# Optimization experiments

Hardware: AMD Instinct MI355X
Metric: run time of the kernel (lower is better)

Reference implementation:

```python
import jax, jax.numpy as jnp
import numpy as np

N, C, H, W = 8, 256, 64, 64  # C == dim_inner

def conv1x1(x, w, b):
    # x: [N,C,H,W], w: [O,C], b: [O]  (1x1 conv == per-pixel matmul)
    return jnp.einsum('oc,nchw->nohw', w, x) + b[None, :, None, None]

def setup_inputs() -> dict:
    key = jax.random.key(0)
    ks = jax.random.split(key, 10)
    s = 1.0 / np.sqrt(C)
    return {
        'x':       jax.random.normal(ks[0], (N, C, H, W), dtype=jnp.float32),
        'w_theta': jax.random.uniform(ks[1], (C, C), jnp.float32, -s, s),
        'b_theta': jax.random.uniform(ks[2], (C,),   jnp.float32, -s, s),
        'w_phi':   jax.random.uniform(ks[3], (C, C), jnp.float32, -s, s),
        'b_phi':   jax.random.uniform(ks[4], (C,),   jnp.float32, -s, s),
        'w_g':     jax.random.uniform(ks[5], (C, C), jnp.float32, -s, s),
        'b_g':     jax.random.uniform(ks[6], (C,),   jnp.float32, -s, s),
        'w_out':   jax.random.uniform(ks[7], (C, C), jnp.float32, -s, s),
        'b_out':   jax.random.uniform(ks[8], (C,),   jnp.float32, -s, s),
        'gamma':   jnp.ones((C,), jnp.float32),
        'beta':    jnp.zeros((C,), jnp.float32),
        'w_gate':  jnp.asarray(0.5, jnp.float32),
    }

def reference(x, w_theta, b_theta, w_phi, b_phi, w_g, b_g, w_out, b_out, gamma, beta, w_gate):
    norm_eps = 1e-5
    x_identity = x
    theta = conv1x1(x, w_theta, b_theta).reshape(N, C, H * W)
    phi   = conv1x1(x, w_phi,   b_phi  ).reshape(N, C, H * W)
    g     = conv1x1(x, w_g,     b_g    ).reshape(N, C, H * W)
    # [N, HW, HW] attention scores
    theta_phi = jnp.einsum('nch,ncp->nhp', theta, phi) * (C ** -0.5)
    theta_phi = jax.nn.softmax(theta_phi, axis=2)
    theta_phi_g = jnp.einsum('nhg,ncg->nch', theta_phi, g).reshape(N, C, H, W)
    p = conv1x1(theta_phi_g, w_out, b_out)
    # BatchNorm2d in training mode: batch stats over (N,H,W), biased var
    mean = p.mean(axis=(0, 2, 3))
    var = p.var(axis=(0, 2, 3))
    p = (p - mean[None, :, None, None]) * jax.lax.rsqrt(var + norm_eps)[None, :, None, None]
    p = p * gamma[None, :, None, None] + beta[None, :, None, None]
    z = (1.0 - w_gate) * x_identity + w_gate * p
    return z
```

## Files before the change

kernel.cpp:

```cpp
#include <hip/hip_runtime.h>

#define N_ 8
#define C_ 256
#define HW_ 4096

typedef __bf16 bf16x8 __attribute__((ext_vector_type(8)));
typedef float f32x4 __attribute__((ext_vector_type(4)));
typedef unsigned short u16x8 __attribute__((ext_vector_type(8)));

#define MFMA(a, b, c) __builtin_amdgcn_mfma_f32_16x16x32_bf16(a, b, c, 0, 0, 0)

static __device__ __forceinline__ unsigned short f2bf(float f) {
    union { float f; unsigned int u; } v; v.f = f;
    unsigned int u = v.u;
    return (unsigned short)((u + 0x7FFFu + ((u >> 16) & 1u)) >> 16);
}

static __device__ __forceinline__ bf16x8 pack_bf8(float4 a, float4 b) {
    u16x8 t;
    t[0] = f2bf(a.x); t[1] = f2bf(a.y); t[2] = f2bf(a.z); t[3] = f2bf(a.w);
    t[4] = f2bf(b.x); t[5] = f2bf(b.y); t[6] = f2bf(b.z); t[7] = f2bf(b.w);
    return __builtin_bit_cast(bf16x8, t);
}

__global__ __launch_bounds__(256) void qkv_kernel(
    const float* __restrict__ x,
    const float* __restrict__ w_theta, const float* __restrict__ b_theta,
    const float* __restrict__ w_phi,   const float* __restrict__ b_phi,
    const float* __restrict__ w_g,     const float* __restrict__ b_g,
    unsigned short* __restrict__ thetaT, unsigned short* __restrict__ phiT,
    unsigned short* __restrict__ gC)
{
    __shared__ unsigned short xT[64 * 264];
    const int tid = threadIdx.x;
    const int hw0 = blockIdx.x * 64;
    const int n   = blockIdx.y;
    const float* xb = x + (size_t)n * C_ * HW_;
    for (int i = 0; i < 16; ++i) {
        int e   = tid + i * 256;
        int c   = e >> 4;
        int hw4 = (e & 15) << 2;
        float4 v = *reinterpret_cast<const float4*>(xb + (size_t)c * HW_ + hw0 + hw4);
        xT[(hw4 + 0) * 264 + c] = f2bf(v.x);
        xT[(hw4 + 1) * 264 + c] = f2bf(v.y);
        xT[(hw4 + 2) * 264 + c] = f2bf(v.z);
        xT[(hw4 + 3) * 264 + c] = f2bf(v.w);
    }
    __syncthreads();

    const int w = tid >> 6, lane = tid & 63;
    const int g16 = lane >> 4, l16 = lane & 15;

    const float* Wp[3] = { w_theta, w_phi, w_g };
    const float* Bp[3] = { b_theta, b_phi, b_g };

    for (int ot = 0; ot < 4; ++ot) {
        const int oB    = ot * 64;
        const int wrow  = oB + w * 16 + l16;
        const int orow0 = oB + w * 16 + g16 * 4;
        #pragma unroll
        for (int wt = 0; wt < 3; ++wt) {
            const float* W = Wp[wt];
            bf16x8 aw[8];
            #pragma unroll
            for (int kk = 0; kk < 8; ++kk) {
                const float* wp = W + (size_t)wrow * C_ + kk * 32 + g16 * 8;
                float4 f0 = *reinterpret_cast<const float4*>(wp);
                float4 f1 = *reinterpret_cast<const float4*>(wp + 4);
                aw[kk] = pack_bf8(f0, f1);
            }
            f32x4 acc[4];
            #pragma unroll
            for (int cb = 0; cb < 4; ++cb) {
                acc[cb][0] = 0.f; acc[cb][1] = 0.f; acc[cb][2] = 0.f; acc[cb][3] = 0.f;
            }
            #pragma unroll
            for (int kk = 0; kk < 8; ++kk) {
                #pragma unroll
                for (int cb = 0; cb < 4; ++cb) {
                    bf16x8 b = *reinterpret_cast<const bf16x8*>(
                        &xT[(cb * 16 + l16) * 264 + kk * 32 + g16 * 8]);
                    acc[cb] = MFMA(aw[kk], b, acc[cb]);
                }
            }
            const float* bp = Bp[wt];
            float bj0 = bp[orow0], bj1 = bp[orow0 + 1], bj2 = bp[orow0 + 2], bj3 = bp[orow0 + 3];
            if (wt == 2) { bj0 = 0.f; bj1 = 0.f; bj2 = 0.f; bj3 = 0.f; }
            if (wt < 2) {
                unsigned short* dst = (wt == 0) ? thetaT : phiT;
                const float sc = (wt == 0) ? 0.0625f : 1.0f;
                #pragma unroll
                for (int cb = 0; cb < 4; ++cb) {
                    int hw = hw0 + cb * 16 + l16;
                    ushort4 pk;
                    pk.x = f2bf((acc[cb][0] + bj0) * sc);
                    pk.y = f2bf((acc[cb][1] + bj1) * sc);
                    pk.z = f2bf((acc[cb][2] + bj2) * sc);
                    pk.w = f2bf((acc[cb][3] + bj3) * sc);
                    *reinterpret_cast<ushort4*>(&dst[((size_t)n * HW_ + hw) * C_ + orow0]) = pk;
                }
            } else {
                #pragma unroll
                for (int cb = 0; cb < 4; ++cb) {
                    int hw = hw0 + cb * 16 + l16;
                    gC[((size_t)n * C_ + orow0 + 0) * HW_ + hw] = f2bf(acc[cb][0]);
                    gC[((size_t)n * C_ + orow0 + 1) * HW_ + hw] = f2bf(acc[cb][1]);
                    gC[((size_t)n * C_ + orow0 + 2) * HW_ + hw] = f2bf(acc[cb][2]);
                    gC[((size_t)n * C_ + orow0 + 3) * HW_ + hw] = f2bf(acc[cb][3]);
                }
            }
        }
    }
}

__global__ __launch_bounds__(256, 2) void attn_kernel(
    const unsigned short* __restrict__ thetaT,
    const unsigned short* __restrict__ phiT,
    const unsigned short* __restrict__ gC,
    unsigned short* __restrict__ tpgT)
{
    __shared__ unsigned short Kl[64 * 264];
    __shared__ unsigned short Vl[256 * 72];
    __shared__ unsigned short Pl[4 * 16 * 72];
    const int tid = threadIdx.x;
    const int h0  = blockIdx.x * 64;
    const int n   = blockIdx.y;
    const int w = tid >> 6, lane = tid & 63, g16 = lane >> 4, l16 = lane & 15;

    bf16x8 q[8];
    {
        const unsigned short* qp = thetaT + ((size_t)n * HW_ + h0 + w * 16 + l16) * C_;
        #pragma unroll
        for (int kk = 0; kk < 8; ++kk)
            q[kk] = *reinterpret_cast<const bf16x8*>(qp + kk * 32 + g16 * 8);
    }
    f32x4 oacc[16];
    #pragma unroll
    for (int i = 0; i < 16; ++i) { oacc[i][0]=0.f; oacc[i][1]=0.f; oacc[i][2]=0.f; oacc[i][3]=0.f; }
    float mj[4] = { -1e30f, -1e30f, -1e30f, -1e30f };
    float lj[4] = { 0.f, 0.f, 0.f, 0.f };

    const unsigned short* Kb = phiT + (size_t)n * HW_ * C_;
    const unsigned short* Vb = gC   + (size_t)n * C_ * HW_;
    unsigned short* Pw = Pl + w * 16 * 72;

    for (int t = 0; t < 64; ++t) {
        __syncthreads();
        for (int i = 0; i < 8; ++i) {
            int e = tid + i * 256;
            int r = e >> 5, c8 = (e & 31) << 3;
            *reinterpret_cast<uint4*>(&Kl[r * 264 + c8]) =
                *reinterpret_cast<const uint4*>(Kb + ((size_t)t * 64 + r) * C_ + c8);
        }
        for (int i = 0; i < 8; ++i) {
            int e = tid + i * 256;
            int c = e >> 3, o8 = (e & 7) << 3;
            *reinterpret_cast<uint4*>(&Vl[c * 72 + o8]) =
                *reinterpret_cast<const uint4*>(Vb + (size_t)c * HW_ + t * 64 + o8);
        }
        __syncthreads();

        f32x4 s[4];
        #pragma unroll
        for (int cb = 0; cb < 4; ++cb) { s[cb][0]=0.f; s[cb][1]=0.f; s[cb][2]=0.f; s[cb][3]=0.f; }
        #pragma unroll
        for (int kk = 0; kk < 8; ++kk) {
            #pragma unroll
            for (int cb = 0; cb < 4; ++cb) {
                bf16x8 b = *reinterpret_cast<const bf16x8*>(
                    &Kl[(cb * 16 + l16) * 264 + kk * 32 + g16 * 8]);
                s[cb] = MFMA(q[kk], b, s[cb]);
            }
        }
        #pragma unroll
        for (int j = 0; j < 4; ++j) {
            float v0 = fmaxf(fmaxf(s[0][j], s[1][j]), fmaxf(s[2][j], s[3][j]));
            v0 = fmaxf(v0, __shfl_xor(v0, 1));
            v0 = fmaxf(v0, __shfl_xor(v0, 2));
            v0 = fmaxf(v0, __shfl_xor(v0, 4));
            v0 = fmaxf(v0, __shfl_xor(v0, 8));
            float mn = fmaxf(mj[j], v0);
            float sc = __expf(mj[j] - mn);
            float rs = 0.f;
            int r = g16 * 4 + j;
            #pragma unroll
            for (int cb = 0; cb < 4; ++cb) {
                float pv = __expf(s[cb][j] - mn);
                rs += pv;
                Pw[r * 72 + cb * 16 + l16] = f2bf(pv);
            }
            rs += __shfl_xor(rs, 1);
            rs += __shfl_xor(rs, 2);
            rs += __shfl_xor(rs, 4);
            rs += __shfl_xor(rs, 8);
            lj[j] = lj[j] * sc + rs;
            mj[j] = mn;
            #pragma unroll
            for (int ncb = 0; ncb < 16; ++ncb) oacc[ncb][j] *= sc;
        }
        #pragma unroll
        for (int k2 = 0; k2 < 2; ++k2) {
            bf16x8 pa = *reinterpret_cast<const bf16x8*>(&Pw[l16 * 72 + k2 * 32 + g16 * 8]);
            #pragma unroll
            for (int ncb = 0; ncb < 16; ++ncb) {
                bf16x8 vb = *reinterpret_cast<const bf16x8*>(
                    &Vl[(ncb * 16 + l16) * 72 + k2 * 32 + g16 * 8]);
                oacc[ncb] = MFMA(pa, vb, oacc[ncb]);
            }
        }
    }
    #pragma unroll
    for (int j = 0; j < 4; ++j) {
        float inv = 1.0f / lj[j];
        int h = h0 + w * 16 + g16 * 4 + j;
        unsigned short* op = tpgT + ((size_t)n * HW_ + h) * C_;
        #pragma unroll
        for (int ncb = 0; ncb < 16; ++ncb)
            op[ncb * 16 + l16] = f2bf(oacc[ncb][j] * inv);
    }
}

__global__ __launch_bounds__(256) void outconv_kernel(
    const unsigned short* __restrict__ tpgT,
    const float* __restrict__ w_out, const float* __restrict__ b_out,
    float* __restrict__ p, float* __restrict__ bnsum, float* __restrict__ bnsumsq)
{
    __shared__ unsigned short Bl[64 * 264];
    const int tid = threadIdx.x;
    const int hw0 = blockIdx.x * 64;
    const int n   = blockIdx.y;
    const unsigned short* Tb = tpgT + (size_t)n * HW_ * C_;
    for (int i = 0; i < 8; ++i) {
        int e = tid + i * 256;
        int r = e >> 5, c8 = (e & 31) << 3;
        *reinterpret_cast<uint4*>(&Bl[r * 264 + c8]) =
            *reinterpret_cast<const uint4*>(Tb + ((size_t)hw0 + r) * C_ + c8);
    }
    __syncthreads();
    const int w = tid >> 6, lane = tid & 63, g16 = lane >> 4, l16 = lane & 15;

    for (int ot = 0; ot < 4; ++ot) {
        const int oB   = ot * 64;
        const int wrow = oB + w * 16 + l16;
        bf16x8 aw[8];
        #pragma unroll
        for (int kk = 0; kk < 8; ++kk) {
            const float* wp = w_out + (size_t)wrow * C_ + kk * 32 + g16 * 8;
            float4 f0 = *reinterpret_cast<const float4*>(wp);
            float4 f1 = *reinterpret_cast<const float4*>(wp + 4);
            aw[kk] = pack_bf8(f0, f1);
        }
        f32x4 acc[4];
        #pragma unroll
        for (int cb = 0; cb < 4; ++cb) { acc[cb][0]=0.f; acc[cb][1]=0.f; acc[cb][2]=0.f; acc[cb][3]=0.f; }
        #pragma unroll
        for (int kk = 0; kk < 8; ++kk) {
            #pragma unroll
            for (int cb = 0; cb < 4; ++cb) {
                bf16x8 b = *reinterpret_cast<const bf16x8*>(
                    &Bl[(cb * 16 + l16) * 264 + kk * 32 + g16 * 8]);
                acc[cb] = MFMA(aw[kk], b, acc[cb]);
            }
        }
        const int orow0 = oB + w * 16 + g16 * 4;
        float bj[4] = { b_out[orow0], b_out[orow0 + 1], b_out[orow0 + 2], b_out[orow0 + 3] };
        float s1[4] = {0.f,0.f,0.f,0.f}, s2[4] = {0.f,0.f,0.f,0.f};
        #pragma unroll
        for (int cb = 0; cb < 4; ++cb) {
            #pragma unroll
            for (int j = 0; j < 4; ++j) {
                float pv = acc[cb][j] + bj[j];
                p[((size_t)n * C_ + orow0 + j) * HW_ + hw0 + cb * 16 + l16] = pv;
                s1[j] += pv;
                s2[j] += pv * pv;
            }
        }
        #pragma unroll
        for (int j = 0; j < 4; ++j) {
            float a1 = s1[j], a2 = s2[j];
            a1 += __shfl_xor(a1, 1); a2 += __shfl_xor(a2, 1);
            a1 += __shfl_xor(a1, 2); a2 += __shfl_xor(a2, 2);
            a1 += __shfl_xor(a1, 4); a2 += __shfl_xor(a2, 4);
            a1 += __shfl_xor(a1, 8); a2 += __shfl_xor(a2, 8);
            if (l16 == 0) {
                atomicAdd(&bnsum[orow0 + j], a1);
                atomicAdd(&bnsumsq[orow0 + j], a2);
            }
        }
    }
}

__global__ void bnfin_kernel(const float* __restrict__ bnsum,
                             const float* __restrict__ bnsumsq,
                             const float* __restrict__ gamma,
                             const float* __restrict__ beta,
                             float* __restrict__ bnscale, float* __restrict__ bnshift)
{
    int c = threadIdx.x;
    const float cnt = (float)(N_ * HW_);
    float mean = bnsum[c] / cnt;
    float var  = bnsumsq[c] / cnt - mean * mean;
    float inv  = rsqrtf(var + 1e-5f);
    float sc   = gamma[c] * inv;
    bnscale[c] = sc;
    bnshift[c] = beta[c] - mean * sc;
}

__global__ __launch_bounds__(256) void final_kernel(
    const float* __restrict__ x, const float* __restrict__ p,
    const float* __restrict__ bnscale, const float* __restrict__ bnshift,
    const float* __restrict__ wgate, float* __restrict__ out)
{
    const float wg = *wgate;
    const float og = 1.0f - wg;
    const int total = N_ * C_ * HW_ / 4;
    for (int e = blockIdx.x * 256 + threadIdx.x; e < total; e += gridDim.x * 256) {
        int c = (e >> 10) & 255;
        float sc = bnscale[c], sh = bnshift[c];
        float4 xv = reinterpret_cast<const float4*>(x)[e];
        float4 pv = reinterpret_cast<const float4*>(p)[e];
        float4 z;
        z.x = og * xv.x + wg * (pv.x * sc + sh);
        z.y = og * xv.y + wg * (pv.y * sc + sh);
        z.z = og * xv.z + wg * (pv.z * sc + sh);
        z.w = og * xv.w + wg * (pv.w * sc + sh);
        reinterpret_cast<float4*>(out)[e] = z;
    }
}

extern "C" void kernel_launch(void* const* d_in, const int* in_sizes, int n_in,
                              void* d_out, int out_size, void* d_ws, size_t ws_size,
                              hipStream_t stream)
{
    (void)in_sizes; (void)n_in; (void)out_size; (void)ws_size;
    const float* x       = (const float*)d_in[0];
    const float* w_theta = (const float*)d_in[1];
    const float* b_theta = (const float*)d_in[2];
    const float* w_phi   = (const float*)d_in[3];
    const float* b_phi   = (const float*)d_in[4];
    const float* w_g     = (const float*)d_in[5];
    const float* b_g     = (const float*)d_in[6];
    const float* w_out   = (const float*)d_in[7];
    const float* b_out   = (const float*)d_in[8];
    const float* gamma   = (const float*)d_in[9];
    const float* beta    = (const float*)d_in[10];
    const float* wgate   = (const float*)d_in[11];
    float* out = (float*)d_out;

    char* ws = (char*)d_ws;
    unsigned short* thetaT = (unsigned short*)(ws + 0);
    unsigned short* phiT   = (unsigned short*)(ws + 16777216);
    unsigned short* gC     = (unsigned short*)(ws + 33554432);
    unsigned short* tpgT   = (unsigned short*)(ws + 50331648);
    float* p       = (float*)(ws + 0);
    float* bnsum   = (float*)(ws + 67108864);
    float* bnsumsq = (float*)(ws + 67108864 + 1024);
    float* bnscale = (float*)(ws + 67108864 + 2048);
    float* bnshift = (float*)(ws + 67108864 + 3072);

    hipMemsetAsync(bnsum, 0, 2048, stream);

    qkv_kernel<<<dim3(64, 8), 256, 0, stream>>>(
        x, w_theta, b_theta, w_phi, b_phi, w_g, b_g, thetaT, phiT, gC);
    attn_kernel<<<dim3(64, 8), 256, 0, stream>>>(thetaT, phiT, gC, tpgT);
    outconv_kernel<<<dim3(64, 8), 256, 0, stream>>>(tpgT, w_out, b_out, p, bnsum, bnsumsq);
    bnfin_kernel<<<1, 256, 0, stream>>>(bnsum, bnsumsq, gamma, beta, bnscale, bnshift);
    final_kernel<<<dim3(2048), 256, 0, stream>>>(x, p, bnscale, bnshift, wgate, out);
}
```

Before: 582.1 us.

## Rewrite attention with 32x32 MFMA, split-KV waves, register-resident P and lazy rescale

The flash-attention kernel moves from 16x16x32 to 32x32x16 bf16 MFMA tiles and computes S transposed, so the probabilities can be packed with v_cvt_pk_bf16 and permlane32 swaps straight into the A operand of the PV MFMA, with no LDS round trip. The four waves are split into two query sub-tiles times two KV halves, each half keeping its own running max and sum, and the halves are merged through LDS at the end. Output rescaling is skipped unless the max grows by more than 8, and the block index is remapped with batch innermost. The aim is higher MFMA efficiency and less LDS and softmax overhead, at the cost of more registers, a final merge step, and some numeric slack from the lazy rescale threshold.

```diff
diff --git a/kernel.cpp b/kernel.cpp
--- a/kernel.cpp
+++ b/kernel.cpp
@@ -6,9 +6,12 @@
 
 typedef __bf16 bf16x8 __attribute__((ext_vector_type(8)));
 typedef float f32x4 __attribute__((ext_vector_type(4)));
+typedef float f32x16 __attribute__((ext_vector_type(16)));
 typedef unsigned short u16x8 __attribute__((ext_vector_type(8)));
-
-#define MFMA(a, b, c) __builtin_amdgcn_mfma_f32_16x16x32_bf16(a, b, c, 0, 0, 0)
+typedef unsigned int uint2v __attribute__((ext_vector_type(2)));
+
+#define MFMA(a, b, c)   __builtin_amdgcn_mfma_f32_16x16x32_bf16(a, b, c, 0, 0, 0)
+#define MFMA32(a, b, c) __builtin_amdgcn_mfma_f32_32x32x16_bf16(a, b, c, 0, 0, 0)
 
 static __device__ __forceinline__ unsigned short f2bf(float f) {
     union { float f; unsigned int u; } v; v.f = f;
@@ -21,6 +24,21 @@
     t[0] = f2bf(a.x); t[1] = f2bf(a.y); t[2] = f2bf(a.z); t[3] = f2bf(a.w);
     t[4] = f2bf(b.x); t[5] = f2bf(b.y); t[6] = f2bf(b.z); t[7] = f2bf(b.w);
     return __builtin_bit_cast(bf16x8, t);
+}
+
+static __device__ __forceinline__ unsigned cvt_pk_bf16(float lo, float hi) {
+    unsigned r;
+    asm("v_cvt_pk_bf16_f32 %0, %1, %2" : "=v"(r) : "v"(lo), "v"(hi));
+    return r;
+}
+
+static __device__ __forceinline__ void plswap(unsigned& a, unsigned& b) {
+#if __has_builtin(__builtin_amdgcn_permlane32_swap)
+    uint2v r = __builtin_amdgcn_permlane32_swap(a, b, false, false);
+    a = r[0]; b = r[1];
+#else
+    asm volatile("v_permlane32_swap_b32 %0, %1" : "+v"(a), "+v"(b));
+#endif
 }
 
 __global__ __launch_bounds__(256) void qkv_kernel(
@@ -119,104 +137,161 @@
     const unsigned short* __restrict__ gC,
     unsigned short* __restrict__ tpgT)
 {
-    __shared__ unsigned short Kl[64 * 264];
-    __shared__ unsigned short Vl[256 * 72];
-    __shared__ unsigned short Pl[4 * 16 * 72];
-    const int tid = threadIdx.x;
-    const int h0  = blockIdx.x * 64;
-    const int n   = blockIdx.y;
-    const int w = tid >> 6, lane = tid & 63, g16 = lane >> 4, l16 = lane & 15;
-
-    bf16x8 q[8];
-    {
-        const unsigned short* qp = thetaT + ((size_t)n * HW_ + h0 + w * 16 + l16) * C_;
-        #pragma unroll
-        for (int kk = 0; kk < 8; ++kk)
-            q[kk] = *reinterpret_cast<const bf16x8*>(qp + kk * 32 + g16 * 8);
-    }
-    f32x4 oacc[16];
-    #pragma unroll
-    for (int i = 0; i < 16; ++i) { oacc[i][0]=0.f; oacc[i][1]=0.f; oacc[i][2]=0.f; oacc[i][3]=0.f; }
-    float mj[4] = { -1e30f, -1e30f, -1e30f, -1e30f };
-    float lj[4] = { 0.f, 0.f, 0.f, 0.f };
+    __shared__ __align__(16) unsigned short smem[2 * 32 * 264 + 2 * 256 * 40];
+    __shared__ float mlds[2][2][32];
+    unsigned short* KlA = smem;
+    unsigned short* KlB = smem + 32 * 264;
+    unsigned short* VlA = smem + 2 * 32 * 264;
+    unsigned short* VlB = VlA + 256 * 40;
+
+    const int tid  = threadIdx.x;
+    const int bid  = blockIdx.x;
+    const int n    = bid & 7;
+    const int q0   = (bid >> 3) * 64;
+    const int w    = tid >> 6, lane = tid & 63;
+    const int l31  = lane & 31;
+    const int hi8  = (lane >> 5) << 3;
+    const int qsub = w & 1, kvhalf = w >> 1;
 
     const unsigned short* Kb = phiT + (size_t)n * HW_ * C_;
     const unsigned short* Vb = gC   + (size_t)n * C_ * HW_;
-    unsigned short* Pw = Pl + w * 16 * 72;
+    const unsigned short* Klh = kvhalf ? KlB : KlA;
+    const unsigned short* Vlh = kvhalf ? VlB : VlA;
+    const int kvbase0 = kvhalf * 2048;
+
+    bf16x8 qf[16];
+    {
+        const unsigned short* qp = thetaT + ((size_t)n * HW_ + q0 + qsub * 32 + l31) * C_;
+        #pragma unroll
+        for (int kk = 0; kk < 16; ++kk)
+            qf[kk] = *reinterpret_cast<const bf16x8*>(qp + kk * 16 + hi8);
+    }
+
+    f32x16 oacc[8];
+    #pragma unroll
+    for (int ncb = 0; ncb < 8; ++ncb)
+        #pragma unroll
+        for (int r = 0; r < 16; ++r) oacc[ncb][r] = 0.f;
+    float m = -1e30f, l = 0.f;
 
     for (int t = 0; t < 64; ++t) {
+        const int kvA = t * 32;
+        const int kvB = 2048 + t * 32;
         __syncthreads();
-        for (int i = 0; i < 8; ++i) {
+        #pragma unroll
+        for (int i = 0; i < 4; ++i) {
             int e = tid + i * 256;
-            int r = e >> 5, c8 = (e & 31) << 3;
-            *reinterpret_cast<uint4*>(&Kl[r * 264 + c8]) =
-                *reinterpret_cast<const uint4*>(Kb + ((size_t)t * 64 + r) * C_ + c8);
-        }
-        for (int i = 0; i < 8; ++i) {
-            int e = tid + i * 256;
-            int c = e >> 3, o8 = (e & 7) << 3;
-            *reinterpret_cast<uint4*>(&Vl[c * 72 + o8]) =
-                *reinterpret_cast<const uint4*>(Vb + (size_t)c * HW_ + t * 64 + o8);
+            int r  = e >> 5, c8 = (e & 31) << 3;
+            *reinterpret_cast<uint4*>(&KlA[r * 264 + c8]) =
+                *reinterpret_cast<const uint4*>(Kb + (size_t)(kvA + r) * C_ + c8);
+            *reinterpret_cast<uint4*>(&KlB[r * 264 + c8]) =
+                *reinterpret_cast<const uint4*>(Kb + (size_t)(kvB + r) * C_ + c8);
+            int c  = e >> 2, o8 = (e & 3) << 3;
+            *reinterpret_cast<uint4*>(&VlA[c * 40 + o8]) =
+                *reinterpret_cast<const uint4*>(Vb + (size_t)c * HW_ + kvA + o8);
+            *reinterpret_cast<uint4*>(&VlB[c * 40 + o8]) =
+                *reinterpret_cast<const uint4*>(Vb + (size_t)c * HW_ + kvB + o8);
         }
         __syncthreads();
 
-        f32x4 s[4];
-        #pragma unroll
-        for (int cb = 0; cb < 4; ++cb) { s[cb][0]=0.f; s[cb][1]=0.f; s[cb][2]=0.f; s[cb][3]=0.f; }
+        f32x16 sA, sB;
+        #pragma unroll
+        for (int r = 0; r < 16; ++r) { sA[r] = 0.f; sB[r] = 0.f; }
         #pragma unroll
         for (int kk = 0; kk < 8; ++kk) {
-            #pragma unroll
-            for (int cb = 0; cb < 4; ++cb) {
-                bf16x8 b = *reinterpret_cast<const bf16x8*>(
-                    &Kl[(cb * 16 + l16) * 264 + kk * 32 + g16 * 8]);
-                s[cb] = MFMA(q[kk], b, s[cb]);
-            }
-        }
-        #pragma unroll
-        for (int j = 0; j < 4; ++j) {
-            float v0 = fmaxf(fmaxf(s[0][j], s[1][j]), fmaxf(s[2][j], s[3][j]));
-            v0 = fmaxf(v0, __shfl_xor(v0, 1));
-            v0 = fmaxf(v0, __shfl_xor(v0, 2));
-            v0 = fmaxf(v0, __shfl_xor(v0, 4));
-            v0 = fmaxf(v0, __shfl_xor(v0, 8));
-            float mn = fmaxf(mj[j], v0);
-            float sc = __expf(mj[j] - mn);
-            float rs = 0.f;
-            int r = g16 * 4 + j;
-            #pragma unroll
-            for (int cb = 0; cb < 4; ++cb) {
-                float pv = __expf(s[cb][j] - mn);
-                rs += pv;
-                Pw[r * 72 + cb * 16 + l16] = f2bf(pv);
-            }
-            rs += __shfl_xor(rs, 1);
-            rs += __shfl_xor(rs, 2);
-            rs += __shfl_xor(rs, 4);
-            rs += __shfl_xor(rs, 8);
-            lj[j] = lj[j] * sc + rs;
-            mj[j] = mn;
-            #pragma unroll
-            for (int ncb = 0; ncb < 16; ++ncb) oacc[ncb][j] *= sc;
-        }
-        #pragma unroll
-        for (int k2 = 0; k2 < 2; ++k2) {
-            bf16x8 pa = *reinterpret_cast<const bf16x8*>(&Pw[l16 * 72 + k2 * 32 + g16 * 8]);
-            #pragma unroll
-            for (int ncb = 0; ncb < 16; ++ncb) {
-                bf16x8 vb = *reinterpret_cast<const bf16x8*>(
-                    &Vl[(ncb * 16 + l16) * 72 + k2 * 32 + g16 * 8]);
-                oacc[ncb] = MFMA(pa, vb, oacc[ncb]);
-            }
-        }
-    }
-    #pragma unroll
-    for (int j = 0; j < 4; ++j) {
-        float inv = 1.0f / lj[j];
-        int h = h0 + w * 16 + g16 * 4 + j;
-        unsigned short* op = tpgT + ((size_t)n * HW_ + h) * C_;
-        #pragma unroll
-        for (int ncb = 0; ncb < 16; ++ncb)
-            op[ncb * 16 + l16] = f2bf(oacc[ncb][j] * inv);
+            bf16x8 af = *reinterpret_cast<const bf16x8*>(&Klh[l31 * 264 + kk * 16 + hi8]);
+            sA = MFMA32(af, qf[kk], sA);
+        }
+        #pragma unroll
+        for (int kk = 8; kk < 16; ++kk) {
+            bf16x8 af = *reinterpret_cast<const bf16x8*>(&Klh[l31 * 264 + kk * 16 + hi8]);
+            sB = MFMA32(af, qf[kk], sB);
+        }
+        f32x16 s = sA + sB;
+
+        float own = s[0];
+        #pragma unroll
+        for (int r = 1; r < 16; ++r) own = fmaxf(own, s[r]);
+        float pmax = fmaxf(own, __shfl_xor(own, 32));
+        if (__any(pmax > m + 8.f)) {
+            float mn = fmaxf(m, pmax);
+            float f  = __expf(m - mn);
+            m = mn; l *= f;
+            #pragma unroll
+            for (int r = 0; r < 16; ++r) {
+                int qr = (r & 3) + 8 * (r >> 2) + (hi8 >> 1);
+                float fr = __shfl(f, qr);
+                #pragma unroll
+                for (int ncb = 0; ncb < 8; ++ncb) oacc[ncb][r] *= fr;
+            }
+        }
+        float lsum = 0.f;
+        #pragma unroll
+        for (int r = 0; r < 16; ++r) {
+            float e = __expf(s[r] - m);
+            lsum += e;
+            s[r] = e;
+        }
+        l += lsum;
+
+        #pragma unroll
+        for (int kk = 0; kk < 2; ++kk) {
+            unsigned w0 = cvt_pk_bf16(s[kk * 8 + 0], s[kk * 8 + 1]);
+            unsigned w1 = cvt_pk_bf16(s[kk * 8 + 2], s[kk * 8 + 3]);
+            unsigned w2 = cvt_pk_bf16(s[kk * 8 + 4], s[kk * 8 + 5]);
+            unsigned w3 = cvt_pk_bf16(s[kk * 8 + 6], s[kk * 8 + 7]);
+            plswap(w0, w2);
+            plswap(w1, w3);
+            uint4 pw; pw.x = w0; pw.y = w1; pw.z = w2; pw.w = w3;
+            bf16x8 pf = __builtin_bit_cast(bf16x8, pw);
+            #pragma unroll
+            for (int ncb = 0; ncb < 8; ++ncb) {
+                bf16x8 vf = *reinterpret_cast<const bf16x8*>(
+                    &Vlh[(ncb * 32 + l31) * 40 + kk * 16 + hi8]);
+                oacc[ncb] = MFMA32(pf, vf, oacc[ncb]);
+            }
+        }
+    }
+
+    float l_tot = l + __shfl_xor(l, 32);
+
+    __syncthreads();
+    float* Obuf = reinterpret_cast<float*>(smem);
+    if (kvhalf == 1) {
+        #pragma unroll
+        for (int r = 0; r < 16; ++r) {
+            int qr = (r & 3) + 8 * (r >> 2) + (hi8 >> 1);
+            #pragma unroll
+            for (int ncb = 0; ncb < 8; ++ncb)
+                Obuf[qsub * 8192 + qr * 256 + ncb * 32 + l31] = oacc[ncb][r];
+        }
+        if (lane < 32) {
+            mlds[qsub][0][l31] = m;
+            mlds[qsub][1][l31] = l_tot;
+        }
+    }
+    __syncthreads();
+    if (kvhalf == 0) {
+        float m2 = mlds[qsub][0][l31];
+        float l2 = mlds[qsub][1][l31];
+        float M  = fmaxf(m, m2);
+        float f1 = __expf(m - M);
+        float f2 = __expf(m2 - M);
+        float Li = 1.0f / (l_tot * f1 + l2 * f2);
+        unsigned short* op = tpgT + ((size_t)n * HW_ + q0 + qsub * 32) * C_;
+        #pragma unroll
+        for (int r = 0; r < 16; ++r) {
+            int qr = (r & 3) + 8 * (r >> 2) + (hi8 >> 1);
+            float f1r = __shfl(f1, qr);
+            float f2r = __shfl(f2, qr);
+            float Lir = __shfl(Li, qr);
+            #pragma unroll
+            for (int ncb = 0; ncb < 8; ++ncb) {
+                float o2 = Obuf[qsub * 8192 + qr * 256 + ncb * 32 + l31];
+                float v  = (oacc[ncb][r] * f1r + o2 * f2r) * Lir;
+                op[(size_t)qr * C_ + ncb * 32 + l31] = f2bf(v);
+            }
+        }
     }
 }
 
@@ -362,7 +437,7 @@
 
     qkv_kernel<<<dim3(64, 8), 256, 0, stream>>>(
         x, w_theta, b_theta, w_phi, b_phi, w_g, b_g, thetaT, phiT, gC);
-    attn_kernel<<<dim3(64, 8), 256, 0, stream>>>(thetaT, phiT, gC, tpgT);
+    attn_kernel<<<dim3(512), 256, 0, stream>>>(thetaT, phiT, gC, tpgT);
     outconv_kernel<<<dim3(64, 8), 256, 0, stream>>>(tpgT, w_out, b_out, p, bnsum, bnsumsq);
     bnfin_kernel<<<1, 256, 0, stream>>>(bnsum, bnsumsq, gamma, beta, bnscale, bnshift);
     final_kernel<<<dim3(2048), 256, 0, stream>>>(x, p, bnscale, bnshift, wgate, out);
```

After: 657.3 us. 1.13x slower.
